# Performance work log

Hardware: AMD Instinct MI355X
Metric: run time of the kernel (lower is better)

Reference implementation:

```python
import jax, jax.numpy as jnp
import numpy as np

H = W = 512
IN_DIM = 3
WIDTH = 64
N_LAYERS = 4
M1 = M2 = 20
FC_DIM = 128
OUT_DIM = 1


def setup_inputs() -> dict:
    key = jax.random.key(0)
    ks = jax.random.split(key, 12)
    s = 1.0 / (WIDTH * WIDTH)
    return {
        "x": jax.random.normal(ks[0], (H, W, IN_DIM), jnp.float32),
        "fc0_w": jax.random.normal(ks[1], (WIDTH, IN_DIM), jnp.float32) * 0.1,
        "fc0_b": jnp.zeros((WIDTH,), jnp.float32),
        "sw1_r": jax.random.normal(ks[2], (N_LAYERS, WIDTH, WIDTH, M1, M2), jnp.float32) * s,
        "sw1_i": jax.random.normal(ks[3], (N_LAYERS, WIDTH, WIDTH, M1, M2), jnp.float32) * s,
        "sw2_r": jax.random.normal(ks[4], (N_LAYERS, WIDTH, WIDTH, M1, M2), jnp.float32) * s,
        "sw2_i": jax.random.normal(ks[5], (N_LAYERS, WIDTH, WIDTH, M1, M2), jnp.float32) * s,
        "conv_w": jax.random.normal(ks[6], (N_LAYERS, WIDTH, WIDTH), jnp.float32) * 0.1,
        "conv_b": jnp.zeros((N_LAYERS, WIDTH), jnp.float32),
        "fc1_w": jax.random.normal(ks[7], (FC_DIM, WIDTH), jnp.float32) * 0.1,
        "fc1_b": jnp.zeros((FC_DIM,), jnp.float32),
        "fc2_w": jax.random.normal(ks[8], (OUT_DIM, FC_DIM), jnp.float32) * 0.1,
        "fc2_b": jnp.zeros((OUT_DIM,), jnp.float32),
    }


def _spectral_conv(v, w1, w2):
    # v: (C, H, W); w1, w2: (C_in, C_out, M1, M2) complex64
    xf = jnp.fft.rfft2(v)  # (C, H, W//2+1) complex64
    out_ft = jnp.zeros((w1.shape[1], H, W // 2 + 1), jnp.complex64)
    top = jnp.einsum("ixy,ioxy->oxy", xf[:, :M1, :M2], w1)
    bot = jnp.einsum("ixy,ioxy->oxy", xf[:, -M1:, :M2], w2)
    out_ft = out_ft.at[:, :M1, :M2].set(top).at[:, -M1:, :M2].set(bot)
    return jnp.fft.irfft2(out_ft, s=(H, W))


def reference(x, fc0_w, fc0_b, sw1_r, sw1_i, sw2_r, sw2_i, conv_w, conv_b,
              fc1_w, fc1_b, fc2_w, fc2_b):
    v = jnp.transpose(x, (2, 0, 1))  # (in_dim, H, W)
    # fc0 applied pointwise over the grid (double_vmap Linear on channel axis)
    v = jnp.einsum("chw,oc->ohw", v, fc0_w) + fc0_b[:, None, None]
    for i in range(N_LAYERS):
        w1 = (sw1_r[i] + 1j * sw1_i[i]).astype(jnp.complex64)
        w2 = (sw2_r[i] + 1j * sw2_i[i]).astype(jnp.complex64)
        x1 = _spectral_conv(v, w1, w2)
        x2 = jnp.einsum("chw,oc->ohw", v, conv_w[i]) + conv_b[i][:, None, None]
        v = jnp.tanh(x1 + x2)
    v = jnp.tanh(jnp.einsum("chw,oc->ohw", v, fc1_w) + fc1_b[:, None, None])
    v = jnp.einsum("chw,oc->ohw", v, fc2_w) + fc2_b[:, None, None]
    return jnp.transpose(v, (1, 2, 0))  # (H, W, out_dim)
```

## Files before the change

### kernel.cpp

```cpp
#include <hip/hip_runtime.h>
#include <math.h>

typedef unsigned short u16;
typedef __attribute__((ext_vector_type(8))) short short8;
typedef __attribute__((ext_vector_type(8))) short bf16x8;
typedef __attribute__((ext_vector_type(4))) unsigned short us4;
typedef __attribute__((ext_vector_type(2))) unsigned short us2;
typedef __attribute__((ext_vector_type(8))) unsigned short us8;
typedef __attribute__((ext_vector_type(4))) float f32x4;

#define NP (512*512)
#define MFMA16 __builtin_amdgcn_mfma_f32_16x16x32_bf16

#define TWH   0u
#define TWL   49152u
#define T2H   98304u
#define T2L   163840u
#define THC2H 229376u
#define THC2L 278528u
#define THS2H 327680u
#define THS2L 376832u
#define THCAH 425984u
#define THCAL 491520u
#define THSAH 557056u
#define THSAL 622592u
#define THSNH 688128u
#define THSNL 753664u
#define CFH   819200u
#define CFL   851968u
#define F1H   884736u
#define F1L   901120u
#define XWH   917504u
#define XWL   4063232u
#define XFP   7208960u
#define YPART 8028160u
#define YRH   8847360u
#define YRL   9011200u
#define YIH   9175040u
#define YIL   9338880u
#define ZH    9502720u
#define ZL    13697024u
#define VH    17891328u
#define VL    51445760u

__device__ __forceinline__ u16 brnd(float x){
    unsigned u = __float_as_uint(x);
    unsigned r = (u + 0x7FFFu + ((u>>16)&1u)) >> 16;
    return (u16)r;
}
__device__ __forceinline__ float fbf(u16 h){ return __uint_as_float(((unsigned)h)<<16); }
__device__ __forceinline__ void bsplit(float x, u16& h, u16& l){
    h = brnd(x); l = brnd(x - fbf(h));
}
__device__ __forceinline__ float tanhfast(float x){
    x = fminf(10.f, fmaxf(-10.f, x));
    float e = __expf(2.f*x);
    return (e-1.f)/(e+1.f);
}

__global__ void k_setup(char* wsb, const float* __restrict__ convw, const float* __restrict__ fc1w){
    int i = blockIdx.x*256 + threadIdx.x;
    const float c2pi = 6.283185307179586f/512.0f;
    if (i < 24576){
        int e=i&7, lane=(i>>3)&63, g=i>>9; int nt=g%3;
        int k = (g/3)*32 + ((lane>>4)<<3) + e;
        int n = nt*16 + (lane&15);
        float v=0.f;
        if(n<40){int kx=n>>1; float a=c2pi*(float)((kx*k)&511); v=(n&1)?-sinf(a):cosf(a);}
        u16 h,l; bsplit(v,h,l);
        ((u16*)(wsb+TWH))[i]=h; ((u16*)(wsb+TWL))[i]=l;
    } else if (i < 57344){
        int j2=i-24576;
        int e=j2&7, lane=(j2>>3)&63, g=j2>>9; int ks=g&1, wt=g>>1;
        int j = ks*32 + ((lane>>4)<<3) + e;
        int w = wt*16 + (lane&15);
        float v=0.f;
        if(j<40){int kx=j>>1; float a=c2pi*(float)((kx*w)&511); v=(j&1)?-sinf(a):cosf(a);}
        u16 h,l; bsplit(v,h,l);
        ((u16*)(wsb+T2H))[j2]=h; ((u16*)(wsb+T2L))[j2]=l;
    } else if (i < 81920){
        int j2 = i-57344;
        int m=j2>>9, hh=j2&511;
        float vc=0.f,vs=0.f;
        if(m<40){int ky=(m<20)?m:(472+m); float a=c2pi*(float)((ky*hh)&511); vc=cosf(a); vs=sinf(a);}
        u16 h,l;
        bsplit(vc,h,l); ((u16*)(wsb+THC2H))[j2]=h; ((u16*)(wsb+THC2L))[j2]=l;
        bsplit(vs,h,l); ((u16*)(wsb+THS2H))[j2]=h; ((u16*)(wsb+THS2L))[j2]=l;
    } else if (i < 114688){
        int j2 = i-81920;
        int hh=j2>>6, m=j2&63;
        float vc=0.f,vs=0.f;
        if(m<40){int ky=(m<20)?m:(472+m); float a=c2pi*(float)((ky*hh)&511); vc=cosf(a); vs=sinf(a);}
        u16 h,l;
        bsplit(vc,h,l);  ((u16*)(wsb+THCAH))[j2]=h; ((u16*)(wsb+THCAL))[j2]=l;
        bsplit(vs,h,l);  ((u16*)(wsb+THSAH))[j2]=h; ((u16*)(wsb+THSAL))[j2]=l;
        bsplit(-vs,h,l); ((u16*)(wsb+THSNH))[j2]=h; ((u16*)(wsb+THSNL))[j2]=l;
    } else {
        int j = i - 114688;
        if (j < 16384){
            int e=j&7, lane=(j>>3)&63, g=j>>9;
            int mt=g&3, ks=(g>>2)&1, L=g>>3;
            int o = mt*16+(lane&15), c = ks*32+((lane>>4)<<3)+e;
            float v = convw[L*4096 + o*64 + c];
            u16 h,l; bsplit(v,h,l);
            ((u16*)(wsb+CFH))[j]=h; ((u16*)(wsb+CFL))[j]=l;
        } else {
            int j2=j-16384;
            int e=j2&7, lane=(j2>>3)&63, g=j2>>9;
            int mt=g&7, ks=g>>3;
            int f = mt*16+(lane&15), c = ks*32+((lane>>4)<<3)+e;
            float v = fc1w[f*64+c];
            u16 h,l; bsplit(v,h,l);
            ((u16*)(wsb+F1H))[j2]=h; ((u16*)(wsb+F1L))[j2]=l;
        }
    }
}

__global__ __launch_bounds__(256) void k_fc0(const float* __restrict__ x,
    const float* __restrict__ w, const float* __restrict__ b,
    u16* __restrict__ vh, u16* __restrict__ vl){
    __shared__ float xs[1024*3];
    __shared__ float ws3[192], bs[64];
    int t = threadIdx.x;
    size_t pb = (size_t)blockIdx.x*1024;
    const float4* xg = (const float4*)(x + pb*3);
    float4* xs4 = (float4*)xs;
    #pragma unroll
    for (int k=0;k<3;k++) xs4[t + k*256] = xg[t + k*256];
    if (t<192) ws3[t]=w[t];
    if (t<64) bs[t]=b[t];
    __syncthreads();
    int p0 = t*4;
    float X0[4],X1[4],X2[4];
    #pragma unroll
    for(int e=0;e<4;e++){X0[e]=xs[(p0+e)*3];X1[e]=xs[(p0+e)*3+1];X2[e]=xs[(p0+e)*3+2];}
    for (int c=0;c<64;c++){
        float w0=ws3[c*3],w1=ws3[c*3+1],w2=ws3[c*3+2],bc=bs[c];
        us4 sh, sl;
        #pragma unroll
        for(int e=0;e<4;e++){
            float v = w0*X0[e]+w1*X1[e]+w2*X2[e]+bc;
            u16 hh,ll; bsplit(v,hh,ll); sh[e]=hh; sl[e]=ll;
        }
        *(us4*)(vh + (size_t)c*NP + pb + p0) = sh;
        *(us4*)(vl + (size_t)c*NP + pb + p0) = sl;
    }
}

__global__ __launch_bounds__(256) void k_f1(const u16* __restrict__ vh, const u16* __restrict__ vl,
    const u16* __restrict__ twh, const u16* __restrict__ twl,
    u16* __restrict__ xwh, u16* __restrict__ xwl){
    int lane = threadIdx.x & 63, wv = threadIdx.x >> 6;
    int r0a = blockIdx.x*128 + wv*16;
    int r1a = r0a + 64;
    int rl = lane&15;
    const u16* ah0 = vh + (size_t)(r0a+rl)*512 + ((lane>>4)<<3);
    const u16* al0 = vl + (size_t)(r0a+rl)*512 + ((lane>>4)<<3);
    const u16* ah1 = vh + (size_t)(r1a+rl)*512 + ((lane>>4)<<3);
    const u16* al1 = vl + (size_t)(r1a+rl)*512 + ((lane>>4)<<3);
    f32x4 acc[2][3];
    #pragma unroll
    for (int tt = 0; tt < 2; ++tt)
        #pragma unroll
        for (int nt = 0; nt < 3; ++nt) acc[tt][nt] = (f32x4){0.f,0.f,0.f,0.f};
    #pragma unroll 2
    for (int kk = 0; kk < 16; ++kk){
        bf16x8 Bh[3], Bl[3];
        #pragma unroll
        for (int nt = 0; nt < 3; ++nt){
            size_t bo = ((size_t)(kk*3+nt)*64 + lane)*8;
            Bh[nt] = *reinterpret_cast<const bf16x8*>(twh + bo);
            Bl[nt] = *reinterpret_cast<const bf16x8*>(twl + bo);
        }
        bf16x8 Ah0 = *reinterpret_cast<const bf16x8*>(ah0 + kk*32);
        bf16x8 Al0 = *reinterpret_cast<const bf16x8*>(al0 + kk*32);
        bf16x8 Ah1 = *reinterpret_cast<const bf16x8*>(ah1 + kk*32);
        bf16x8 Al1 = *reinterpret_cast<const bf16x8*>(al1 + kk*32);
        #pragma unroll
        for (int nt = 0; nt < 3; ++nt){
            acc[0][nt] = MFMA16(Ah0, Bh[nt], acc[0][nt], 0,0,0);
            acc[0][nt] = MFMA16(Ah0, Bl[nt], acc[0][nt], 0,0,0);
            acc[0][nt] = MFMA16(Al0, Bh[nt], acc[0][nt], 0,0,0);
            acc[1][nt] = MFMA16(Ah1, Bh[nt], acc[1][nt], 0,0,0);
            acc[1][nt] = MFMA16(Ah1, Bl[nt], acc[1][nt], 0,0,0);
            acc[1][nt] = MFMA16(Al1, Bh[nt], acc[1][nt], 0,0,0);
        }
    }
    int colj = lane&15;
    #pragma unroll
    for (int tt = 0; tt < 2; ++tt){
        int r0 = (tt ? r1a : r0a) + ((lane>>4)<<2);
        int c = r0>>9, h0 = r0&511;
        #pragma unroll
        for (int nt = 0; nt < 3; ++nt){
            int j = nt*16 + colj;
            us4 uh, ul;
            #pragma unroll
            for (int rg = 0; rg < 4; ++rg){
                u16 hh,ll; bsplit(acc[tt][nt][rg],hh,ll); uh[rg]=hh; ul[rg]=ll;
            }
            size_t off = ((size_t)j*64 + c)*512 + h0;
            *(us4*)(xwh + off) = uh;
            *(us4*)(xwl + off) = ul;
        }
    }
}

__global__ __launch_bounds__(256) void k_f2(const char* __restrict__ wsb, float* __restrict__ xfP){
    int b = blockIdx.x;
    int kx = b/6, r = b%6, mt = r>>1, kh = r&1;
    int lane = threadIdx.x&63, wv = threadIdx.x>>6;
    const u16* thch=(const u16*)(wsb+THC2H); const u16* thcl=(const u16*)(wsb+THC2L);
    const u16* thsh=(const u16*)(wsb+THS2H); const u16* thsl=(const u16*)(wsb+THS2L);
    const u16* xwh=(const u16*)(wsb+XWH);   const u16* xwl=(const u16*)(wsb+XWL);
    f32x4 aA=(f32x4){0,0,0,0}, aB=aA, aC=aA, aD=aA;
    int g8 = (lane>>4)<<3;
    int mrow = lane&15;
    int cB = wv*16 + (lane&15);
    size_t bre = ((size_t)(2*kx)*64 + cB)*512;
    size_t bim = ((size_t)(2*kx+1)*64 + cB)*512;
    for (int kk = kh*8; kk < kh*8+8; ++kk){
        int hof = kk*32 + g8;
        bf16x8 XRh = *reinterpret_cast<const bf16x8*>(xwh + bre + hof);
        bf16x8 XRl = *reinterpret_cast<const bf16x8*>(xwl + bre + hof);
        bf16x8 XIh = *reinterpret_cast<const bf16x8*>(xwh + bim + hof);
        bf16x8 XIl = *reinterpret_cast<const bf16x8*>(xwl + bim + hof);
        size_t ao = (size_t)(mt*16+mrow)*512 + hof;
        bf16x8 Ch = *reinterpret_cast<const bf16x8*>(thch+ao);
        bf16x8 Cl = *reinterpret_cast<const bf16x8*>(thcl+ao);
        bf16x8 Sh = *reinterpret_cast<const bf16x8*>(thsh+ao);
        bf16x8 Sl = *reinterpret_cast<const bf16x8*>(thsl+ao);
        aA=MFMA16(Ch,XRh,aA,0,0,0); aA=MFMA16(Ch,XRl,aA,0,0,0); aA=MFMA16(Cl,XRh,aA,0,0,0);
        aB=MFMA16(Sh,XIh,aB,0,0,0); aB=MFMA16(Sh,XIl,aB,0,0,0); aB=MFMA16(Sl,XIh,aB,0,0,0);
        aC=MFMA16(Ch,XIh,aC,0,0,0); aC=MFMA16(Ch,XIl,aC,0,0,0); aC=MFMA16(Cl,XIh,aC,0,0,0);
        aD=MFMA16(Sh,XRh,aD,0,0,0); aD=MFMA16(Sh,XRl,aD,0,0,0); aD=MFMA16(Sl,XRh,aD,0,0,0);
    }
    #pragma unroll
    for (int rg=0;rg<4;rg++){
        int m = mt*16 + ((lane>>4)<<2) + rg;
        if (m < 40){
            float re = aA[rg]+aB[rg];
            float im = aC[rg]-aD[rg];
            size_t xo = ((size_t)kh*64 + cB)*1600 + (size_t)(m*20+kx)*2;
            xfP[xo] = re; xfP[xo+1] = im;
        }
    }
}

__global__ __launch_bounds__(256) void k_mix(const float* __restrict__ w1r,const float* __restrict__ w1i,
    const float* __restrict__ w2r,const float* __restrict__ w2i,
    const float* __restrict__ xfP, float* __restrict__ ypart){
    __shared__ float xs[2][800];
    int b = blockIdx.x;
    int iseg = b>>7, half = (b>>6)&1, o = b&63;
    int t = threadIdx.x;
    const float* wr = (half? w2r : w1r) + o*400;
    const float* wi = (half? w2i : w1i) + o*400;
    const float* xp0 = xfP + half*800;
    const float* xp1 = xfP + (size_t)64*1600 + half*800;
    int i0 = iseg*32;
    {
        const float* a = xp0 + (size_t)i0*1600; const float* c = xp1 + (size_t)i0*1600;
        xs[0][t]=a[t]+c[t]; xs[0][t+256]=a[t+256]+c[t+256];
        if (t<288) xs[0][t+512]=a[t+512]+c[t+512];
    }
    int p1 = t, p2 = t+256; bool has2 = (p2<400);
    float ar1=0,ai1=0,ar2=0,ai2=0;
    size_t wof = (size_t)i0*25600;
    float wAr1=wr[wof+p1], wAi1=wi[wof+p1];
    float wAr2=0,wAi2=0;
    if(has2){ wAr2=wr[wof+p2]; wAi2=wi[wof+p2]; }
    __syncthreads();
    for (int ii=0; ii<32; ++ii){
        int cur = ii&1;
        if (ii<31){
            int i = i0+ii+1;
            const float* a = xp0 + (size_t)i*1600; const float* c = xp1 + (size_t)i*1600;
            float* d = xs[cur^1];
            d[t]=a[t]+c[t]; d[t+256]=a[t+256]+c[t+256];
            if(t<288) d[t+512]=a[t+512]+c[t+512];
        }
        float wBr1=0,wBi1=0,wBr2=0,wBi2=0;
        if (ii<31){
            size_t wo2 = (size_t)(i0+ii+1)*25600;
            wBr1=wr[wo2+p1]; wBi1=wi[wo2+p1];
            if(has2){ wBr2=wr[wo2+p2]; wBi2=wi[wo2+p2]; }
        }
        float xr=xs[cur][2*p1], xi=xs[cur][2*p1+1];
        ar1 += xr*wAr1 - xi*wAi1; ai1 += xr*wAi1 + xi*wAr1;
        if (has2){
            float xr2=xs[cur][2*p2], xi2=xs[cur][2*p2+1];
            ar2 += xr2*wAr2 - xi2*wAi2; ai2 += xr2*wAi2 + xi2*wAr2;
        }
        wAr1=wBr1; wAi1=wBi1; wAr2=wBr2; wAi2=wBi2;
        __syncthreads();
    }
    int mode1 = half*400 + p1;
    size_t y1 = ((size_t)(iseg*800 + mode1)*64 + o)*2;
    ypart[y1]=ar1; ypart[y1+1]=ai1;
    if (has2){
        int mode2 = half*400 + p2;
        size_t y2 = ((size_t)(iseg*800 + mode2)*64 + o)*2;
        ypart[y2]=ar2; ypart[y2+1]=ai2;
    }
}

__global__ void k_mixred(const float* __restrict__ ypart, char* wsb){
    int g = blockIdx.x*256+threadIdx.x;
    int m = g&63, o=(g>>6)&63, kx=g>>12;
    float vr=0.f, vi=0.f;
    if (m<40){
        int mode = m*20+kx;
        size_t i0 = ((size_t)mode*64+o)*2;
        size_t i1 = ((size_t)(800+mode)*64+o)*2;
        float sc = (kx==0?1.f:2.f)*(1.f/262144.f);
        vr = (ypart[i0]+ypart[i1])*sc;
        vi = (ypart[i0+1]+ypart[i1+1])*sc;
    }
    u16 h,l; size_t yo = ((size_t)kx*64+o)*64+m;
    bsplit(vr,h,l); ((u16*)(wsb+YRH))[yo]=h; ((u16*)(wsb+YRL))[yo]=l;
    bsplit(vi,h,l); ((u16*)(wsb+YIH))[yo]=h; ((u16*)(wsb+YIL))[yo]=l;
}

__global__ __launch_bounds__(128) void k_i1(const char* __restrict__ wsb,
    u16* __restrict__ zh, u16* __restrict__ zl){
    int b = blockIdx.x; int kx = b>>4, hb = b&15;
    int lane = threadIdx.x&63, wv = threadIdx.x>>6;
    const u16* thcAh=(const u16*)(wsb+THCAH); const u16* thcAl=(const u16*)(wsb+THCAL);
    const u16* thsAh=(const u16*)(wsb+THSAH); const u16* thsAl=(const u16*)(wsb+THSAL);
    const u16* thsnh=(const u16*)(wsb+THSNH); const u16* thsnl=(const u16*)(wsb+THSNL);
    const u16* yrh=(const u16*)(wsb+YRH); const u16* yrl=(const u16*)(wsb+YRL);
    const u16* yih=(const u16*)(wsb+YIH); const u16* yil=(const u16*)(wsb+YIL);
    f32x4 aR[4], aI[4];
    #pragma unroll
    for(int nt=0;nt<4;nt++){aR[nt]=(f32x4){0,0,0,0}; aI[nt]=aR[nt];}
    int g8 = (lane>>4)<<3;
    int hrow = hb*32 + wv*16 + (lane&15);
    #pragma unroll
    for (int ks=0; ks<2; ++ks){
        size_t ao = (size_t)hrow*64 + ks*32 + g8;
        bf16x8 Ch=*reinterpret_cast<const bf16x8*>(thcAh+ao);
        bf16x8 Cl=*reinterpret_cast<const bf16x8*>(thcAl+ao);
        bf16x8 Sh=*reinterpret_cast<const bf16x8*>(thsAh+ao);
        bf16x8 Sl=*reinterpret_cast<const bf16x8*>(thsAl+ao);
        bf16x8 Nh=*reinterpret_cast<const bf16x8*>(thsnh+ao);
        bf16x8 Nl=*reinterpret_cast<const bf16x8*>(thsnl+ao);
        #pragma unroll
        for (int nt=0; nt<4; ++nt){
            int o = nt*16+(lane&15);
            size_t bo = ((size_t)kx*64+o)*64 + ks*32 + g8;
            bf16x8 Rh=*reinterpret_cast<const bf16x8*>(yrh+bo);
            bf16x8 Rl=*reinterpret_cast<const bf16x8*>(yrl+bo);
            bf16x8 Ih=*reinterpret_cast<const bf16x8*>(yih+bo);
            bf16x8 Il=*reinterpret_cast<const bf16x8*>(yil+bo);
            aR[nt]=MFMA16(Ch,Rh,aR[nt],0,0,0); aR[nt]=MFMA16(Ch,Rl,aR[nt],0,0,0); aR[nt]=MFMA16(Cl,Rh,aR[nt],0,0,0);
            aR[nt]=MFMA16(Nh,Ih,aR[nt],0,0,0); aR[nt]=MFMA16(Nh,Il,aR[nt],0,0,0); aR[nt]=MFMA16(Nl,Ih,aR[nt],0,0,0);
            aI[nt]=MFMA16(Sh,Rh,aI[nt],0,0,0); aI[nt]=MFMA16(Sh,Rl,aI[nt],0,0,0); aI[nt]=MFMA16(Sl,Rh,aI[nt],0,0,0);
            aI[nt]=MFMA16(Ch,Ih,aI[nt],0,0,0); aI[nt]=MFMA16(Ch,Il,aI[nt],0,0,0); aI[nt]=MFMA16(Cl,Ih,aI[nt],0,0,0);
        }
    }
    #pragma unroll
    for (int nt=0;nt<4;nt++)
        #pragma unroll
        for (int rg=0;rg<4;rg++){
            int h = hb*32 + wv*16 + ((lane>>4)<<2) + rg;
            int o = nt*16+(lane&15);
            size_t za = ((size_t)h*64+o)*64 + 2*kx;
            u16 h1,l1,h2,l2;
            bsplit(aR[nt][rg],h1,l1); bsplit(aI[nt][rg],h2,l2);
            us2 sh={h1,h2}, sl={l1,l2};
            *(us2*)(zh+za)=sh; *(us2*)(zl+za)=sl;
        }
}

#define SWZ(c,p) ((c) ^ (((p)&7)<<3))
__global__ __launch_bounds__(256) void k_sct(u16* __restrict__ vh, u16* __restrict__ vl,
    const char* __restrict__ wsb, int L, const float* __restrict__ cb,
    const u16* __restrict__ zh, const u16* __restrict__ zl){
    __shared__ __align__(16) char smem[17408];
    u16* sh_ = (u16*)smem;
    u16* sl_ = (u16*)(smem + 8192);
    unsigned* so_ = (unsigned*)smem;
    int t = threadIdx.x, lane = t&63, wv = t>>6;
    int h = blockIdx.x>>3, pb = (blockIdx.x&7)<<6;
    size_t gbase = (size_t)h*512 + pb;
    const u16* cfh=(const u16*)(wsb+CFH); const u16* cfl=(const u16*)(wsb+CFL);
    const u16* t2h=(const u16*)(wsb+T2H); const u16* t2l=(const u16*)(wsb+T2L);
    int g = lane>>4;
    int colp = wv*16 + (lane&15);
    int wt = (pb>>4) + wv;
    int cst = t>>2, p0s=(t&3)<<4;
    short8 a0 = *(const short8*)(vh + (size_t)cst*NP + gbase + p0s);
    short8 a1 = *(const short8*)(vh + (size_t)cst*NP + gbase + p0s+8);
    short8 b0 = *(const short8*)(vl + (size_t)cst*NP + gbase + p0s);
    short8 b1 = *(const short8*)(vl + (size_t)cst*NP + gbase + p0s+8);
    bf16x8 cA0[4][2], zA0[4][2], tB0[2];
    #pragma unroll
    for (int mt=0;mt<4;mt++){
        size_t fo = (size_t)(((L*2+0)*4+mt)*64 + lane)*8;
        cA0[mt][0] = *reinterpret_cast<const bf16x8*>(cfh+fo);
        cA0[mt][1] = *reinterpret_cast<const bf16x8*>(cfl+fo);
        size_t ao = (((size_t)h*64 + mt*16+(lane&15))*64) + (g<<3);
        zA0[mt][0] = *reinterpret_cast<const bf16x8*>(zh+ao);
        zA0[mt][1] = *reinterpret_cast<const bf16x8*>(zl+ao);
    }
    {
        size_t bo = ((size_t)(wt*2+0)*64 + lane)*8;
        tB0[0] = *reinterpret_cast<const bf16x8*>(t2h+bo);
        tB0[1] = *reinterpret_cast<const bf16x8*>(t2l+bo);
    }
    #pragma unroll
    for (int e=0;e<8;e++){
        sh_[(p0s+e)*64 + SWZ(cst,p0s+e)] = (u16)a0[e];
        sh_[(p0s+8+e)*64 + SWZ(cst,p0s+8+e)] = (u16)a1[e];
        sl_[(p0s+e)*64 + SWZ(cst,p0s+e)] = (u16)b0[e];
        sl_[(p0s+8+e)*64 + SWZ(cst,p0s+8+e)] = (u16)b1[e];
    }
    __syncthreads();
    f32x4 acc[4];
    #pragma unroll
    for (int mt=0;mt<4;mt++) acc[mt]=(f32x4){0,0,0,0};
    {
        int so = colp*64 + ((g ^ (colp&7))<<3);
        bf16x8 Bh = *reinterpret_cast<const bf16x8*>(sh_+so);
        bf16x8 Bl = *reinterpret_cast<const bf16x8*>(sl_+so);
        #pragma unroll
        for (int mt=0;mt<4;mt++){
            acc[mt]=MFMA16(cA0[mt][0],Bh,acc[mt],0,0,0);
            acc[mt]=MFMA16(cA0[mt][0],Bl,acc[mt],0,0,0);
            acc[mt]=MFMA16(cA0[mt][1],Bh,acc[mt],0,0,0);
        }
    }
    bf16x8 cA1[4][2], zA1[4][2], tB1[2];
    #pragma unroll
    for (int mt=0;mt<4;mt++){
        size_t fo = (size_t)(((L*2+1)*4+mt)*64 + lane)*8;
        cA1[mt][0] = *reinterpret_cast<const bf16x8*>(cfh+fo);
        cA1[mt][1] = *reinterpret_cast<const bf16x8*>(cfl+fo);
        size_t ao = (((size_t)h*64 + mt*16+(lane&15))*64) + 32 + (g<<3);
        zA1[mt][0] = *reinterpret_cast<const bf16x8*>(zh+ao);
        zA1[mt][1] = *reinterpret_cast<const bf16x8*>(zl+ao);
    }
    {
        size_t bo = ((size_t)(wt*2+1)*64 + lane)*8;
        tB1[0] = *reinterpret_cast<const bf16x8*>(t2h+bo);
        tB1[1] = *reinterpret_cast<const bf16x8*>(t2l+bo);
    }
    #pragma unroll
    for (int mt=0;mt<4;mt++){
        acc[mt]=MFMA16(zA0[mt][0],tB0[0],acc[mt],0,0,0);
        acc[mt]=MFMA16(zA0[mt][0],tB0[1],acc[mt],0,0,0);
        acc[mt]=MFMA16(zA0[mt][1],tB0[0],acc[mt],0,0,0);
    }
    {
        int so = colp*64 + (((4+g) ^ (colp&7))<<3);
        bf16x8 Bh = *reinterpret_cast<const bf16x8*>(sh_+so);
        bf16x8 Bl = *reinterpret_cast<const bf16x8*>(sl_+so);
        #pragma unroll
        for (int mt=0;mt<4;mt++){
            acc[mt]=MFMA16(cA1[mt][0],Bh,acc[mt],0,0,0);
            acc[mt]=MFMA16(cA1[mt][0],Bl,acc[mt],0,0,0);
            acc[mt]=MFMA16(cA1[mt][1],Bh,acc[mt],0,0,0);
        }
    }
    #pragma unroll
    for (int mt=0;mt<4;mt++){
        acc[mt]=MFMA16(zA1[mt][0],tB1[0],acc[mt],0,0,0);
        acc[mt]=MFMA16(zA1[mt][0],tB1[1],acc[mt],0,0,0);
        acc[mt]=MFMA16(zA1[mt][1],tB1[0],acc[mt],0,0,0);
    }
    __syncthreads();
    #pragma unroll
    for (int mt=0;mt<4;mt++){
        float4 cbv = *reinterpret_cast<const float4*>(cb + mt*16 + (g<<2));
        float cba[4] = {cbv.x, cbv.y, cbv.z, cbv.w};
        #pragma unroll
        for (int rg=0;rg<4;rg++){
            int o = mt*16 + (g<<2) + rg;
            float val = tanhfast(acc[mt][rg] + cba[rg]);
            u16 hh,ll; bsplit(val,hh,ll);
            so_[o*68 + colp] = (unsigned)hh | ((unsigned)ll<<16);
        }
    }
    __syncthreads();
    {
        int o = t>>2, p0 = (t&3)<<4;
        const uint4* sp = reinterpret_cast<const uint4*>(so_ + o*68 + p0);
        uint4 u0 = sp[0], u1 = sp[1], u2 = sp[2], u3 = sp[3];
        us8 h0, h1, l0, l1;
        h0[0]=(u16)u0.x; l0[0]=(u16)(u0.x>>16);
        h0[1]=(u16)u0.y; l0[1]=(u16)(u0.y>>16);
        h0[2]=(u16)u0.z; l0[2]=(u16)(u0.z>>16);
        h0[3]=(u16)u0.w; l0[3]=(u16)(u0.w>>16);
        h0[4]=(u16)u1.x; l0[4]=(u16)(u1.x>>16);
        h0[5]=(u16)u1.y; l0[5]=(u16)(u1.y>>16);
        h0[6]=(u16)u1.z; l0[6]=(u16)(u1.z>>16);
        h0[7]=(u16)u1.w; l0[7]=(u16)(u1.w>>16);
        h1[0]=(u16)u2.x; l1[0]=(u16)(u2.x>>16);
        h1[1]=(u16)u2.y; l1[1]=(u16)(u2.y>>16);
        h1[2]=(u16)u2.z; l1[2]=(u16)(u2.z>>16);
        h1[3]=(u16)u2.w; l1[3]=(u16)(u2.w>>16);
        h1[4]=(u16)u3.x; l1[4]=(u16)(u3.x>>16);
        h1[5]=(u16)u3.y; l1[5]=(u16)(u3.y>>16);
        h1[6]=(u16)u3.z; l1[6]=(u16)(u3.z>>16);
        h1[7]=(u16)u3.w; l1[7]=(u16)(u3.w>>16);
        size_t go = (size_t)o*NP + gbase + p0;
        *(us8*)(vh+go)   = h0;
        *(us8*)(vh+go+8) = h1;
        *(us8*)(vl+go)   = l0;
        *(us8*)(vl+go+8) = l1;
    }
}

__global__ __launch_bounds__(256) void k_fc12(const u16* __restrict__ vh, const u16* __restrict__ vl,
    const char* __restrict__ wsb, const float* __restrict__ b1,
    const float* __restrict__ w2, const float* __restrict__ b2, float* __restrict__ out){
    __shared__ u16 sh_[4096];
    __shared__ u16 sl_[4096];
    int t = threadIdx.x, lane = t&63, wv = t>>6;
    size_t pb = (size_t)blockIdx.x*64;
    {
        int c = t>>2, p0=(t&3)<<4;
        short8 a0 = *(const short8*)(vh + (size_t)c*NP + pb + p0);
        short8 a1 = *(const short8*)(vh + (size_t)c*NP + pb + p0+8);
        short8 b0 = *(const short8*)(vl + (size_t)c*NP + pb + p0);
        short8 b1 = *(const short8*)(vl + (size_t)c*NP + pb + p0+8);
        #pragma unroll
        for (int e=0;e<8;e++){
            sh_[(p0+e)*64 + SWZ(c,p0+e)] = (u16)a0[e];
            sh_[(p0+8+e)*64 + SWZ(c,p0+8+e)] = (u16)a1[e];
            sl_[(p0+e)*64 + SWZ(c,p0+e)] = (u16)b0[e];
            sl_[(p0+8+e)*64 + SWZ(c,p0+8+e)] = (u16)b1[e];
        }
    }
    __syncthreads();
    f32x4 acc[8];
    #pragma unroll
    for (int mt=0;mt<8;mt++) acc[mt]=(f32x4){0,0,0,0};
    int colp = wv*16 + (lane&15);
    int g = lane>>4;
    const u16* f1h=(const u16*)(wsb+F1H); const u16* f1l=(const u16*)(wsb+F1L);
    #pragma unroll
    for (int ks=0;ks<2;ks++){
        bf16x8 A[8][2];
        #pragma unroll
        for (int mt=0;mt<8;mt++){
            size_t fo = (size_t)((ks*8+mt)*64 + lane)*8;
            A[mt][0] = *reinterpret_cast<const bf16x8*>(f1h+fo);
            A[mt][1] = *reinterpret_cast<const bf16x8*>(f1l+fo);
        }
        int o8 = ks*4+g;
        int so = colp*64 + ((o8 ^ (colp&7))<<3);
        bf16x8 Bh = *reinterpret_cast<const bf16x8*>(sh_+so);
        bf16x8 Bl = *reinterpret_cast<const bf16x8*>(sl_+so);
        #pragma unroll
        for (int mt=0;mt<8;mt++){
            acc[mt]=MFMA16(A[mt][0],Bh,acc[mt],0,0,0);
            acc[mt]=MFMA16(A[mt][0],Bl,acc[mt],0,0,0);
            acc[mt]=MFMA16(A[mt][1],Bh,acc[mt],0,0,0);
        }
    }
    float s = 0.f;
    #pragma unroll
    for (int mt=0;mt<8;mt++)
        #pragma unroll
        for (int rg=0;rg<4;rg++){
            int f = mt*16 + (g<<2) + rg;
            s += w2[f] * tanhfast(acc[mt][rg] + b1[f]);
        }
    s += __shfl_xor(s, 16);
    s += __shfl_xor(s, 32);
    if (lane < 16) out[pb + wv*16 + lane] = s + b2[0];
}

extern "C" void kernel_launch(void* const* d_in, const int* in_sizes, int n_in,
                              void* d_out, int out_size, void* d_ws, size_t ws_size,
                              hipStream_t stream) {
    const float* x     = (const float*)d_in[0];
    const float* fc0w  = (const float*)d_in[1];
    const float* fc0b  = (const float*)d_in[2];
    const float* sw1r  = (const float*)d_in[3];
    const float* sw1i  = (const float*)d_in[4];
    const float* sw2r  = (const float*)d_in[5];
    const float* sw2i  = (const float*)d_in[6];
    const float* convw = (const float*)d_in[7];
    const float* convb = (const float*)d_in[8];
    const float* fc1w  = (const float*)d_in[9];
    const float* fc1b  = (const float*)d_in[10];
    const float* fc2w  = (const float*)d_in[11];
    const float* fc2b  = (const float*)d_in[12];
    char* wsb = (char*)d_ws;
    float* out = (float*)d_out;

    u16* twh = (u16*)(wsb+TWH); u16* twl = (u16*)(wsb+TWL);
    u16* xwh = (u16*)(wsb+XWH); u16* xwl = (u16*)(wsb+XWL);
    float* xfP = (float*)(wsb+XFP);
    float* ypart = (float*)(wsb+YPART);
    u16* zh = (u16*)(wsb+ZH); u16* zl = (u16*)(wsb+ZL);
    u16* vh = (u16*)(wsb+VH); u16* vl = (u16*)(wsb+VL);

    k_setup<<<544, 256, 0, stream>>>(wsb, convw, fc1w);
    k_fc0<<<256, 256, 0, stream>>>(x, fc0w, fc0b, vh, vl);
    for (int L = 0; L < 4; ++L){
        size_t so = (size_t)L * 64 * 64 * 400;
        k_f1<<<256, 256, 0, stream>>>(vh, vl, twh, twl, xwh, xwl);
        k_f2<<<120, 256, 0, stream>>>(wsb, xfP);
        k_mix<<<256, 256, 0, stream>>>(sw1r+so, sw1i+so, sw2r+so, sw2i+so, xfP, ypart);
        k_mixred<<<320, 256, 0, stream>>>(ypart, wsb);
        k_i1<<<320, 128, 0, stream>>>(wsb, zh, zl);
        k_sct<<<4096, 256, 0, stream>>>(vh, vl, wsb, L, convb + (size_t)L*64, zh, zl);
    }
    k_fc12<<<4096, 256, 0, stream>>>(vh, vl, wsb, fc1b, fc2w, fc2b, out);
}
```

Before: 727.6 us.

## Remap block indices across XCDs, split mix work into more blocks, separate sct LDS buffers

Block IDs in k_f1, k_sct and k_fc12 are permuted so that consecutive hardware block IDs, which are dealt round-robin across the 8 XCDs, map to contiguous row/pixel chunks on each XCD. This aims to improve L2 locality. k_mix now launches twice as many blocks, each handling 200 modes per thread group instead of 400, which raises parallelism but duplicates the shared xfP staging. k_sct gives its output staging its own LDS region, which removes a __syncthreads but raises LDS use per block and may lower occupancy.

```diff
diff --git a/kernel.cpp b/kernel.cpp
--- a/kernel.cpp
+++ b/kernel.cpp
@@ -150,8 +150,9 @@
 __global__ __launch_bounds__(256) void k_f1(const u16* __restrict__ vh, const u16* __restrict__ vl,
     const u16* __restrict__ twh, const u16* __restrict__ twl,
     u16* __restrict__ xwh, u16* __restrict__ xwl){
+    int bid = ((blockIdx.x & 7) << 5) | (blockIdx.x >> 3);
     int lane = threadIdx.x & 63, wv = threadIdx.x >> 6;
-    int r0a = blockIdx.x*128 + wv*16;
+    int r0a = bid*128 + wv*16;
     int r1a = r0a + 64;
     int rl = lane&15;
     const u16* ah0 = vh + (size_t)(r0a+rl)*512 + ((lane>>4)<<3);
@@ -252,7 +253,7 @@
     const float* __restrict__ xfP, float* __restrict__ ypart){
     __shared__ float xs[2][800];
     int b = blockIdx.x;
-    int iseg = b>>7, half = (b>>6)&1, o = b&63;
+    int iseg = b>>8, half = (b>>7)&1, o = (b>>1)&63, mh = b&1;
     int t = threadIdx.x;
     const float* wr = (half? w2r : w1r) + o*400;
     const float* wi = (half? w2i : w1i) + o*400;
@@ -264,12 +265,11 @@
         xs[0][t]=a[t]+c[t]; xs[0][t+256]=a[t+256]+c[t+256];
         if (t<288) xs[0][t+512]=a[t+512]+c[t+512];
     }
-    int p1 = t, p2 = t+256; bool has2 = (p2<400);
-    float ar1=0,ai1=0,ar2=0,ai2=0;
+    bool act = t < 200;
+    int p1 = mh*200 + (act ? t : 199);
+    float ar1=0,ai1=0;
     size_t wof = (size_t)i0*25600;
     float wAr1=wr[wof+p1], wAi1=wi[wof+p1];
-    float wAr2=0,wAi2=0;
-    if(has2){ wAr2=wr[wof+p2]; wAi2=wi[wof+p2]; }
     __syncthreads();
     for (int ii=0; ii<32; ++ii){
         int cur = ii&1;
@@ -280,28 +280,20 @@
             d[t]=a[t]+c[t]; d[t+256]=a[t+256]+c[t+256];
             if(t<288) d[t+512]=a[t+512]+c[t+512];
         }
-        float wBr1=0,wBi1=0,wBr2=0,wBi2=0;
+        float wBr1=0,wBi1=0;
         if (ii<31){
             size_t wo2 = (size_t)(i0+ii+1)*25600;
             wBr1=wr[wo2+p1]; wBi1=wi[wo2+p1];
-            if(has2){ wBr2=wr[wo2+p2]; wBi2=wi[wo2+p2]; }
         }
         float xr=xs[cur][2*p1], xi=xs[cur][2*p1+1];
         ar1 += xr*wAr1 - xi*wAi1; ai1 += xr*wAi1 + xi*wAr1;
-        if (has2){
-            float xr2=xs[cur][2*p2], xi2=xs[cur][2*p2+1];
-            ar2 += xr2*wAr2 - xi2*wAi2; ai2 += xr2*wAi2 + xi2*wAr2;
-        }
-        wAr1=wBr1; wAi1=wBi1; wAr2=wBr2; wAi2=wBi2;
+        wAr1=wBr1; wAi1=wBi1;
         __syncthreads();
     }
-    int mode1 = half*400 + p1;
-    size_t y1 = ((size_t)(iseg*800 + mode1)*64 + o)*2;
-    ypart[y1]=ar1; ypart[y1+1]=ai1;
-    if (has2){
-        int mode2 = half*400 + p2;
-        size_t y2 = ((size_t)(iseg*800 + mode2)*64 + o)*2;
-        ypart[y2]=ar2; ypart[y2+1]=ai2;
+    if (act){
+        int mode1 = half*400 + p1;
+        size_t y1 = ((size_t)(iseg*800 + mode1)*64 + o)*2;
+        ypart[y1]=ar1; ypart[y1+1]=ai1;
     }
 }
 
@@ -377,12 +369,12 @@
 __global__ __launch_bounds__(256) void k_sct(u16* __restrict__ vh, u16* __restrict__ vl,
     const char* __restrict__ wsb, int L, const float* __restrict__ cb,
     const u16* __restrict__ zh, const u16* __restrict__ zl){
-    __shared__ __align__(16) char smem[17408];
-    u16* sh_ = (u16*)smem;
-    u16* sl_ = (u16*)(smem + 8192);
-    unsigned* so_ = (unsigned*)smem;
+    __shared__ u16 sh_[4096];
+    __shared__ u16 sl_[4096];
+    __shared__ unsigned so_[64*68];
+    int bid = ((blockIdx.x & 7) << 9) | (blockIdx.x >> 3);
     int t = threadIdx.x, lane = t&63, wv = t>>6;
-    int h = blockIdx.x>>3, pb = (blockIdx.x&7)<<6;
+    int h = bid>>3, pb = (bid&7)<<6;
     size_t gbase = (size_t)h*512 + pb;
     const u16* cfh=(const u16*)(wsb+CFH); const u16* cfl=(const u16*)(wsb+CFL);
     const u16* t2h=(const u16*)(wsb+T2H); const u16* t2l=(const u16*)(wsb+T2L);
@@ -469,7 +461,6 @@
         acc[mt]=MFMA16(zA1[mt][0],tB1[1],acc[mt],0,0,0);
         acc[mt]=MFMA16(zA1[mt][1],tB1[0],acc[mt],0,0,0);
     }
-    __syncthreads();
     #pragma unroll
     for (int mt=0;mt<4;mt++){
         float4 cbv = *reinterpret_cast<const float4*>(cb + mt*16 + (g<<2));
@@ -517,8 +508,9 @@
     const float* __restrict__ w2, const float* __restrict__ b2, float* __restrict__ out){
     __shared__ u16 sh_[4096];
     __shared__ u16 sl_[4096];
+    int bid = ((blockIdx.x & 7) << 9) | (blockIdx.x >> 3);
     int t = threadIdx.x, lane = t&63, wv = t>>6;
-    size_t pb = (size_t)blockIdx.x*64;
+    size_t pb = (size_t)bid*64;
     {
         int c = t>>2, p0=(t&3)<<4;
         short8 a0 = *(const short8*)(vh + (size_t)c*NP + pb + p0);
@@ -605,7 +597,7 @@
         size_t so = (size_t)L * 64 * 64 * 400;
         k_f1<<<256, 256, 0, stream>>>(vh, vl, twh, twl, xwh, xwl);
         k_f2<<<120, 256, 0, stream>>>(wsb, xfP);
-        k_mix<<<256, 256, 0, stream>>>(sw1r+so, sw1i+so, sw2r+so, sw2i+so, xfP, ypart);
+        k_mix<<<512, 256, 0, stream>>>(sw1r+so, sw1i+so, sw2r+so, sw2i+so, xfP, ypart);
         k_mixred<<<320, 256, 0, stream>>>(ypart, wsb);
         k_i1<<<320, 128, 0, stream>>>(wsb, zh, zl);
         k_sct<<<4096, 256, 0, stream>>>(vh, vl, wsb, L, convb + (size_t)L*64, zh, zl);
```

After: 746.1 us. 1.03x slower.
